# Kernel optimization log

Measured on AMD Instinct MI355X. Metric: run time of the kernel, lower is better.

The kernel has to match this reference:

```python
import jax, jax.numpy as jnp
import numpy as np

ALPHA = 32
R = 16
SCALING = ALPHA / R  # 2.0


def setup_inputs() -> dict:
    key = jax.random.key(0)
    k1, k2, k3, k4 = jax.random.split(key, 4)
    B_, S, D = 4, 2048, 4096
    H, r, O = 8, R, 4096
    x = jax.random.normal(k1, (B_, S, D), dtype=jnp.float32)
    A = jax.random.normal(k2, (H, r, D), dtype=jnp.float32) * 0.02   # down-proj per head
    Bm = jax.random.normal(k3, (H, O, r), dtype=jnp.float32) * 0.02  # up-proj per head
    Wr = jax.random.normal(k4, (H, D), dtype=jnp.float32) * 0.02     # router weight
    br = jnp.zeros((H,), dtype=jnp.float32)                          # router bias
    return {"x": x, "A": A, "B": Bm, "Wr": Wr, "br": br}


def reference(x, A, B, Wr, br):
    H = A.shape[0]
    # Router: logits [b, s, h], scores scaled by num_heads
    router_logits = jnp.einsum('bsd,hd->bsh', x, Wr) + br
    scores = H * jax.nn.softmax(router_logits, axis=-1)
    # Per-head low-rank projection: [b, s, h, r]
    low = jnp.einsum('bsd,hrd->bshr', x, A)
    # Fused up-projection + router-weighted combine over heads: [b, s, o]
    out = jnp.einsum('bshr,hor,bsh->bso', low, B, scores)
    return SCALING * out
```

## Files before the change

kernel.cpp:

```cpp
#include <hip/hip_runtime.h>
#include <math.h>

#define D_DIM 4096
#define O_DIM 4096
#define KSPLIT 8

typedef __attribute__((ext_vector_type(8))) short short8;
typedef __attribute__((ext_vector_type(4))) float floatx4;

__device__ inline unsigned short f2bf(float f) {
    union { float f; unsigned u; } v; v.f = f;
    unsigned r = v.u + 0x7FFF + ((v.u >> 16) & 1);
    return (unsigned short)(r >> 16);
}

__global__ __launch_bounds__(256) void k0a_prepW1(const float* __restrict__ A,
                                                  const float* __restrict__ Wr,
                                                  unsigned short* __restrict__ W1bf) {
    int e = (blockIdx.x * 256 + threadIdx.x) * 4;
    int row = e >> 12;
    int col = e & 4095;
    float4 v;
    if (row < 128)      v = *(const float4*)(A + (size_t)row * D_DIM + col);
    else if (row < 136) v = *(const float4*)(Wr + (size_t)(row - 128) * D_DIM + col);
    else                v = make_float4(0.f, 0.f, 0.f, 0.f);
    ushort4 o; o.x = f2bf(v.x); o.y = f2bf(v.y); o.z = f2bf(v.z); o.w = f2bf(v.w);
    *(ushort4*)(W1bf + e) = o;
}

__global__ __launch_bounds__(256) void k0b_prepBt(const float* __restrict__ B,
                                                  unsigned short* __restrict__ Btbf) {
    int e = (blockIdx.x * 256 + threadIdx.x) * 4;
    int o = e >> 7;
    int k = e & 127;
    int h = k >> 4;
    int r = k & 15;
    float4 v = *(const float4*)(B + (size_t)h * (O_DIM * 16) + (size_t)o * 16 + r);
    ushort4 w; w.x = f2bf(v.x); w.y = f2bf(v.y); w.z = f2bf(v.z); w.w = f2bf(v.w);
    *(ushort4*)(Btbf + e) = w;
}

__global__ __launch_bounds__(256) void k1_gemm1(const float* __restrict__ X,
                                                const unsigned short* __restrict__ W1bf,
                                                float* __restrict__ P) {
    __shared__ short Xs[64][72];
    __shared__ short Ws[144][72];
    const int kslice = blockIdx.x & (KSPLIT - 1);
    const int mblk   = blockIdx.x >> 3;
    const int m0     = mblk * 64;
    const int kbase  = kslice * (D_DIM / KSPLIT);
    const int tid  = threadIdx.x;
    const int wave = tid >> 6;
    const int lane = tid & 63;
    const int lrow = lane & 15;
    const int quad = lane >> 4;

    floatx4 acc[9];
    #pragma unroll
    for (int n = 0; n < 9; ++n) acc[n] = (floatx4)(0.f);

    for (int it = 0; it < (D_DIM / KSPLIT) / 64; ++it) {
        const int k0c = kbase + it * 64;
        #pragma unroll
        for (int i = 0; i < 4; ++i) {
            int e   = tid + i * 256;
            int row = e >> 4;
            int c4  = e & 15;
            float4 v = *(const float4*)(X + (size_t)(m0 + row) * D_DIM + k0c + c4 * 4);
            ushort4 o; o.x = f2bf(v.x); o.y = f2bf(v.y); o.z = f2bf(v.z); o.w = f2bf(v.w);
            *(ushort4*)&Xs[row][c4 * 4] = o;
        }
        #pragma unroll
        for (int i = 0; i < 5; ++i) {
            int e = tid + i * 256;
            if (e < 1152) {
                int row = e >> 3;
                int c8  = e & 7;
                uint4 v = *(const uint4*)(W1bf + (size_t)row * D_DIM + k0c + c8 * 8);
                *(uint4*)&Ws[row][c8 * 8] = v;
            }
        }
        __syncthreads();
        #pragma unroll
        for (int ks = 0; ks < 2; ++ks) {
            const int koff = ks * 32 + quad * 8;
            short8 a = *(const short8*)&Xs[wave * 16 + lrow][koff];
            #pragma unroll
            for (int n = 0; n < 9; ++n) {
                short8 b = *(const short8*)&Ws[n * 16 + lrow][koff];
                acc[n] = __builtin_amdgcn_mfma_f32_16x16x32_bf16(a, b, acc[n], 0, 0, 0);
            }
        }
        __syncthreads();
    }

    float* Pk = P + (size_t)kslice * (8192 * 144);
    #pragma unroll
    for (int n = 0; n < 9; ++n) {
        #pragma unroll
        for (int reg = 0; reg < 4; ++reg) {
            int row = m0 + wave * 16 + quad * 4 + reg;
            int col = n * 16 + lrow;
            Pk[(size_t)row * 144 + col] = acc[n][reg];
        }
    }
}

__global__ __launch_bounds__(256) void k15_reduce_softmax(const float* __restrict__ P,
                                                          const float* __restrict__ br,
                                                          unsigned short* __restrict__ W2) {
    __shared__ float S[16][148];
    const int t0  = blockIdx.x * 16;
    const int tid = threadIdx.x;
    #pragma unroll
    for (int i = 0; i < 3; ++i) {
        int e = tid + i * 256;
        if (e < 576) {
            int row = e / 36;
            int c4  = e - row * 36;
            size_t off = (size_t)(t0 + row) * 144 + c4 * 4;
            float4 s = *(const float4*)(P + off);
            #pragma unroll
            for (int p = 1; p < KSPLIT; ++p) {
                float4 v = *(const float4*)(P + (size_t)p * (8192 * 144) + off);
                s.x += v.x; s.y += v.y; s.z += v.z; s.w += v.w;
            }
            *(float4*)&S[row][c4 * 4] = s;
        }
    }
    __syncthreads();
    if (tid < 16) {
        float l[8]; float m = -1e30f;
        #pragma unroll
        for (int h = 0; h < 8; ++h) { l[h] = S[tid][128 + h] + br[h]; m = fmaxf(m, l[h]); }
        float s = 0.f;
        #pragma unroll
        for (int h = 0; h < 8; ++h) { l[h] = __expf(l[h] - m); s += l[h]; }
        float inv = 16.0f / s;
        #pragma unroll
        for (int h = 0; h < 8; ++h) S[tid][136 + h] = l[h] * inv;
    }
    __syncthreads();
    #pragma unroll
    for (int i = 0; i < 2; ++i) {
        int e   = tid + i * 256;
        int tok = e >> 5;
        int c4  = e & 31;
        int col = c4 * 4;
        float sc = S[tok][136 + (col >> 4)];
        ushort4 o;
        o.x = f2bf(S[tok][col + 0] * sc);
        o.y = f2bf(S[tok][col + 1] * sc);
        o.z = f2bf(S[tok][col + 2] * sc);
        o.w = f2bf(S[tok][col + 3] * sc);
        *(ushort4*)(W2 + (size_t)(t0 + tok) * 128 + col) = o;
    }
}

__global__ __launch_bounds__(256) void k2_gemm2(const unsigned short* __restrict__ W2,
                                                const unsigned short* __restrict__ Btbf,
                                                float* __restrict__ out) {
    __shared__ short Bs[128][136];
    const int nblk = blockIdx.x & 31;
    const int mblk = blockIdx.x >> 5;
    const int m0 = mblk * 128, n0 = nblk * 128;
    const int tid  = threadIdx.x;
    const int wave = tid >> 6;
    const int lane = tid & 63;
    const int lrow = lane & 15;
    const int quad = lane >> 4;

    #pragma unroll
    for (int i = 0; i < 8; ++i) {
        int e   = tid + i * 256;
        int row = e >> 4;
        int c8  = e & 15;
        *(uint4*)&Bs[row][c8 * 8] = *(const uint4*)(Btbf + (size_t)(n0 + row) * 128 + c8 * 8);
    }
    __syncthreads();

    floatx4 acc[2][8];
    #pragma unroll
    for (int i = 0; i < 2; ++i)
        #pragma unroll
        for (int n = 0; n < 8; ++n) acc[i][n] = (floatx4)(0.f);

    #pragma unroll
    for (int ks = 0; ks < 4; ++ks) {
        const int koff = ks * 32 + quad * 8;
        short8 a[2];
        #pragma unroll
        for (int i = 0; i < 2; ++i)
            a[i] = *(const short8*)(W2 + (size_t)(m0 + wave * 32 + i * 16 + lrow) * 128 + koff);
        #pragma unroll
        for (int n = 0; n < 8; ++n) {
            short8 b = *(const short8*)&Bs[n * 16 + lrow][koff];
            #pragma unroll
            for (int i = 0; i < 2; ++i)
                acc[i][n] = __builtin_amdgcn_mfma_f32_16x16x32_bf16(a[i], b, acc[i][n], 0, 0, 0);
        }
    }

    #pragma unroll
    for (int i = 0; i < 2; ++i) {
        #pragma unroll
        for (int n = 0; n < 8; ++n) {
            #pragma unroll
            for (int reg = 0; reg < 4; ++reg) {
                int row = m0 + wave * 32 + i * 16 + quad * 4 + reg;
                int col = n0 + n * 16 + lrow;
                __builtin_nontemporal_store(acc[i][n][reg], out + (size_t)row * O_DIM + col);
            }
        }
    }
}

extern "C" void kernel_launch(void* const* d_in, const int* in_sizes, int n_in,
                              void* d_out, int out_size, void* d_ws, size_t ws_size,
                              hipStream_t stream) {
    const float* x  = (const float*)d_in[0];
    const float* A  = (const float*)d_in[1];
    const float* B  = (const float*)d_in[2];
    const float* Wr = (const float*)d_in[3];
    const float* br = (const float*)d_in[4];
    float* out = (float*)d_out;

    float* ws = (float*)d_ws;
    float*          P     = ws;
    unsigned short* W2    = (unsigned short*)(ws + 9437184);
    unsigned short* W1bf  = (unsigned short*)(ws + 9437184 + 524288);
    unsigned short* Btbf  = (unsigned short*)(ws + 9437184 + 524288 + 294912);

    k0a_prepW1<<<dim3(576), dim3(256), 0, stream>>>(A, Wr, W1bf);
    k0b_prepBt<<<dim3(512), dim3(256), 0, stream>>>(B, Btbf);
    k1_gemm1<<<dim3(128 * KSPLIT), dim3(256), 0, stream>>>(x, W1bf, P);
    k15_reduce_softmax<<<dim3(512), dim3(256), 0, stream>>>(P, br, W2);
    k2_gemm2<<<dim3(64 * 32), dim3(256), 0, stream>>>(W2, Btbf, out);
}
```

Measured before the change: 289.2 us.

## Fuse router GEMM, softmax and up-projection into one per-token-block kernel

Replaces the split-K GEMM1, global partial-sum reduction and separate GEMM2 with a single kernel. Each 512-thread block owns 16 tokens, its 8 waves split K, and the partial sums are reduced in shared memory before the softmax-scaled weights feed the up-projection. Output is staged through LDS so it can be written with vectorized nontemporal stores. The two prep kernels are merged into one launch. This removes the large fp32 partial buffer round-trip and two launches. In exchange, operands are read directly from global memory without LDS tiling, which raises L2 traffic for W1 and B. Each block also reads a shared 16-token x tile, which may under-use the MFMA units.

```diff
diff --git a/kernel.cpp b/kernel.cpp
--- a/kernel.cpp
+++ b/kernel.cpp
@@ -1,9 +1,9 @@
 #include <hip/hip_runtime.h>
+#include <hip/hip_bf16.h>
 #include <math.h>
 
 #define D_DIM 4096
 #define O_DIM 4096
-#define KSPLIT 8
 
 typedef __attribute__((ext_vector_type(8))) short short8;
 typedef __attribute__((ext_vector_type(4))) float floatx4;
@@ -14,203 +14,153 @@
     return (unsigned short)(r >> 16);
 }
 
-__global__ __launch_bounds__(256) void k0a_prepW1(const float* __restrict__ A,
-                                                  const float* __restrict__ Wr,
-                                                  unsigned short* __restrict__ W1bf) {
-    int e = (blockIdx.x * 256 + threadIdx.x) * 4;
-    int row = e >> 12;
-    int col = e & 4095;
-    float4 v;
-    if (row < 128)      v = *(const float4*)(A + (size_t)row * D_DIM + col);
-    else if (row < 136) v = *(const float4*)(Wr + (size_t)(row - 128) * D_DIM + col);
-    else                v = make_float4(0.f, 0.f, 0.f, 0.f);
-    ushort4 o; o.x = f2bf(v.x); o.y = f2bf(v.y); o.z = f2bf(v.z); o.w = f2bf(v.w);
-    *(ushort4*)(W1bf + e) = o;
+__device__ inline unsigned cvt2(float lo, float hi) {
+    __hip_bfloat162 h2 = __float22bfloat162_rn(make_float2(lo, hi));
+    union { __hip_bfloat162 h; unsigned u; } c; c.h = h2;
+    return c.u;
 }
 
-__global__ __launch_bounds__(256) void k0b_prepBt(const float* __restrict__ B,
-                                                  unsigned short* __restrict__ Btbf) {
-    int e = (blockIdx.x * 256 + threadIdx.x) * 4;
-    int o = e >> 7;
-    int k = e & 127;
-    int h = k >> 4;
-    int r = k & 15;
-    float4 v = *(const float4*)(B + (size_t)h * (O_DIM * 16) + (size_t)o * 16 + r);
-    ushort4 w; w.x = f2bf(v.x); w.y = f2bf(v.y); w.z = f2bf(v.z); w.w = f2bf(v.w);
-    *(ushort4*)(Btbf + e) = w;
+__global__ __launch_bounds__(256) void k0_prep(const float* __restrict__ A,
+                                               const float* __restrict__ Wr,
+                                               const float* __restrict__ B,
+                                               unsigned short* __restrict__ W1bf,
+                                               unsigned short* __restrict__ Btbf) {
+    if (blockIdx.x < 576) {
+        int e = (blockIdx.x * 256 + threadIdx.x) * 4;
+        int row = e >> 12;
+        int col = e & 4095;
+        float4 v;
+        if (row < 128)      v = *(const float4*)(A + (size_t)row * D_DIM + col);
+        else if (row < 136) v = *(const float4*)(Wr + (size_t)(row - 128) * D_DIM + col);
+        else                v = make_float4(0.f, 0.f, 0.f, 0.f);
+        ushort4 o; o.x = f2bf(v.x); o.y = f2bf(v.y); o.z = f2bf(v.z); o.w = f2bf(v.w);
+        *(ushort4*)(W1bf + e) = o;
+    } else {
+        int e = ((blockIdx.x - 576) * 256 + threadIdx.x) * 4;
+        int o = e >> 7;
+        int k = e & 127;
+        int h = k >> 4;
+        int r = k & 15;
+        float4 v = *(const float4*)(B + (size_t)h * (O_DIM * 16) + (size_t)o * 16 + r);
+        ushort4 w; w.x = f2bf(v.x); w.y = f2bf(v.y); w.z = f2bf(v.z); w.w = f2bf(v.w);
+        *(ushort4*)(Btbf + e) = w;
+    }
 }
 
-__global__ __launch_bounds__(256) void k1_gemm1(const float* __restrict__ X,
-                                                const unsigned short* __restrict__ W1bf,
-                                                float* __restrict__ P) {
-    __shared__ short Xs[64][72];
-    __shared__ short Ws[144][72];
-    const int kslice = blockIdx.x & (KSPLIT - 1);
-    const int mblk   = blockIdx.x >> 3;
-    const int m0     = mblk * 64;
-    const int kbase  = kslice * (D_DIM / KSPLIT);
+__global__ __launch_bounds__(512, 4) void kf_fused(const float* __restrict__ X,
+                                                   const unsigned short* __restrict__ W1bf,
+                                                   const unsigned short* __restrict__ Btbf,
+                                                   const float* __restrict__ br,
+                                                   float* __restrict__ out) {
+    __shared__ float Sred[8][16][144];
+    __shared__ unsigned short W2s[16][132];
     const int tid  = threadIdx.x;
     const int wave = tid >> 6;
     const int lane = tid & 63;
     const int lrow = lane & 15;
     const int quad = lane >> 4;
+    const int m0   = blockIdx.x * 16;
 
+    const int kb = wave * 512;
     floatx4 acc[9];
     #pragma unroll
     for (int n = 0; n < 9; ++n) acc[n] = (floatx4)(0.f);
 
-    for (int it = 0; it < (D_DIM / KSPLIT) / 64; ++it) {
-        const int k0c = kbase + it * 64;
+    const float*          xrow  = X    + (size_t)(m0 + lrow) * D_DIM + kb + quad * 8;
+    const unsigned short* wbase = W1bf + (size_t)lrow * D_DIM + kb + quad * 8;
+
+    #pragma unroll 2
+    for (int ks = 0; ks < 16; ++ks) {
+        float4 x0 = *(const float4*)(xrow + ks * 32);
+        float4 x1 = *(const float4*)(xrow + ks * 32 + 4);
+        union { unsigned u[4]; short8 s; } a;
+        a.u[0] = cvt2(x0.x, x0.y); a.u[1] = cvt2(x0.z, x0.w);
+        a.u[2] = cvt2(x1.x, x1.y); a.u[3] = cvt2(x1.z, x1.w);
         #pragma unroll
-        for (int i = 0; i < 4; ++i) {
-            int e   = tid + i * 256;
-            int row = e >> 4;
-            int c4  = e & 15;
-            float4 v = *(const float4*)(X + (size_t)(m0 + row) * D_DIM + k0c + c4 * 4);
-            ushort4 o; o.x = f2bf(v.x); o.y = f2bf(v.y); o.z = f2bf(v.z); o.w = f2bf(v.w);
-            *(ushort4*)&Xs[row][c4 * 4] = o;
+        for (int n = 0; n < 9; ++n) {
+            short8 b = *(const short8*)(wbase + (size_t)n * (16 * D_DIM) + ks * 32);
+            acc[n] = __builtin_amdgcn_mfma_f32_16x16x32_bf16(a.s, b, acc[n], 0, 0, 0);
         }
-        #pragma unroll
-        for (int i = 0; i < 5; ++i) {
-            int e = tid + i * 256;
-            if (e < 1152) {
-                int row = e >> 3;
-                int c8  = e & 7;
-                uint4 v = *(const uint4*)(W1bf + (size_t)row * D_DIM + k0c + c8 * 8);
-                *(uint4*)&Ws[row][c8 * 8] = v;
-            }
-        }
-        __syncthreads();
-        #pragma unroll
-        for (int ks = 0; ks < 2; ++ks) {
-            const int koff = ks * 32 + quad * 8;
-            short8 a = *(const short8*)&Xs[wave * 16 + lrow][koff];
-            #pragma unroll
-            for (int n = 0; n < 9; ++n) {
-                short8 b = *(const short8*)&Ws[n * 16 + lrow][koff];
-                acc[n] = __builtin_amdgcn_mfma_f32_16x16x32_bf16(a, b, acc[n], 0, 0, 0);
-            }
-        }
-        __syncthreads();
     }
 
-    float* Pk = P + (size_t)kslice * (8192 * 144);
     #pragma unroll
-    for (int n = 0; n < 9; ++n) {
+    for (int n = 0; n < 9; ++n)
         #pragma unroll
-        for (int reg = 0; reg < 4; ++reg) {
-            int row = m0 + wave * 16 + quad * 4 + reg;
-            int col = n * 16 + lrow;
-            Pk[(size_t)row * 144 + col] = acc[n][reg];
-        }
-    }
-}
+        for (int reg = 0; reg < 4; ++reg)
+            Sred[wave][quad * 4 + reg][n * 16 + lrow] = acc[n][reg];
+    __syncthreads();
 
-__global__ __launch_bounds__(256) void k15_reduce_softmax(const float* __restrict__ P,
-                                                          const float* __restrict__ br,
-                                                          unsigned short* __restrict__ W2) {
-    __shared__ float S[16][148];
-    const int t0  = blockIdx.x * 16;
-    const int tid = threadIdx.x;
-    #pragma unroll
-    for (int i = 0; i < 3; ++i) {
-        int e = tid + i * 256;
-        if (e < 576) {
-            int row = e / 36;
-            int c4  = e - row * 36;
-            size_t off = (size_t)(t0 + row) * 144 + c4 * 4;
-            float4 s = *(const float4*)(P + off);
-            #pragma unroll
-            for (int p = 1; p < KSPLIT; ++p) {
-                float4 v = *(const float4*)(P + (size_t)p * (8192 * 144) + off);
-                s.x += v.x; s.y += v.y; s.z += v.z; s.w += v.w;
-            }
-            *(float4*)&S[row][c4 * 4] = s;
-        }
+    for (int idx = tid; idx < 2304; idx += 512) {
+        int row = idx / 144;
+        int col = idx - row * 144;
+        float s = Sred[0][row][col];
+        #pragma unroll
+        for (int p = 1; p < 8; ++p) s += Sred[p][row][col];
+        Sred[0][row][col] = s;
     }
     __syncthreads();
+
     if (tid < 16) {
         float l[8]; float m = -1e30f;
         #pragma unroll
-        for (int h = 0; h < 8; ++h) { l[h] = S[tid][128 + h] + br[h]; m = fmaxf(m, l[h]); }
+        for (int h = 0; h < 8; ++h) { l[h] = Sred[0][tid][128 + h] + br[h]; m = fmaxf(m, l[h]); }
         float s = 0.f;
         #pragma unroll
         for (int h = 0; h < 8; ++h) { l[h] = __expf(l[h] - m); s += l[h]; }
         float inv = 16.0f / s;
         #pragma unroll
-        for (int h = 0; h < 8; ++h) S[tid][136 + h] = l[h] * inv;
-    }
-    __syncthreads();
-    #pragma unroll
-    for (int i = 0; i < 2; ++i) {
-        int e   = tid + i * 256;
-        int tok = e >> 5;
-        int c4  = e & 31;
-        int col = c4 * 4;
-        float sc = S[tok][136 + (col >> 4)];
-        ushort4 o;
-        o.x = f2bf(S[tok][col + 0] * sc);
-        o.y = f2bf(S[tok][col + 1] * sc);
-        o.z = f2bf(S[tok][col + 2] * sc);
-        o.w = f2bf(S[tok][col + 3] * sc);
-        *(ushort4*)(W2 + (size_t)(t0 + tok) * 128 + col) = o;
-    }
-}
-
-__global__ __launch_bounds__(256) void k2_gemm2(const unsigned short* __restrict__ W2,
-                                                const unsigned short* __restrict__ Btbf,
-                                                float* __restrict__ out) {
-    __shared__ short Bs[128][136];
-    const int nblk = blockIdx.x & 31;
-    const int mblk = blockIdx.x >> 5;
-    const int m0 = mblk * 128, n0 = nblk * 128;
-    const int tid  = threadIdx.x;
-    const int wave = tid >> 6;
-    const int lane = tid & 63;
-    const int lrow = lane & 15;
-    const int quad = lane >> 4;
-
-    #pragma unroll
-    for (int i = 0; i < 8; ++i) {
-        int e   = tid + i * 256;
-        int row = e >> 4;
-        int c8  = e & 15;
-        *(uint4*)&Bs[row][c8 * 8] = *(const uint4*)(Btbf + (size_t)(n0 + row) * 128 + c8 * 8);
+        for (int h = 0; h < 8; ++h) Sred[0][tid][136 + h] = l[h] * inv;
     }
     __syncthreads();
 
-    floatx4 acc[2][8];
+    {
+        int row = tid >> 5;
+        int c   = (tid & 31) * 4;
+        float sc = Sred[0][row][136 + (c >> 4)];
+        float4 v = *(const float4*)&Sred[0][row][c];
+        ushort4 o;
+        o.x = f2bf(v.x * sc); o.y = f2bf(v.y * sc);
+        o.z = f2bf(v.z * sc); o.w = f2bf(v.w * sc);
+        *(ushort4*)&W2s[row][c] = o;
+    }
+    __syncthreads();
+
+    float* bounce = &Sred[0][0][0] + wave * (16 * 132);
+
+    short8 afr[4];
     #pragma unroll
-    for (int i = 0; i < 2; ++i)
+    for (int ks = 0; ks < 4; ++ks)
+        afr[ks] = *(const short8*)&W2s[lrow][ks * 32 + quad * 8];
+
+    const int nb = wave * 512;
+    for (int nc = 0; nc < 4; ++nc) {
+        const int n0c = nb + nc * 128;
+        floatx4 acc2[8];
         #pragma unroll
-        for (int n = 0; n < 8; ++n) acc[i][n] = (floatx4)(0.f);
+        for (int n = 0; n < 8; ++n) acc2[n] = (floatx4)(0.f);
 
-    #pragma unroll
-    for (int ks = 0; ks < 4; ++ks) {
-        const int koff = ks * 32 + quad * 8;
-        short8 a[2];
         #pragma unroll
-        for (int i = 0; i < 2; ++i)
-            a[i] = *(const short8*)(W2 + (size_t)(m0 + wave * 32 + i * 16 + lrow) * 128 + koff);
+        for (int ks = 0; ks < 4; ++ks)
+            #pragma unroll
+            for (int n = 0; n < 8; ++n) {
+                short8 b = *(const short8*)(Btbf + (size_t)(n0c + n * 16 + lrow) * 128 + ks * 32 + quad * 8);
+                acc2[n] = __builtin_amdgcn_mfma_f32_16x16x32_bf16(afr[ks], b, acc2[n], 0, 0, 0);
+            }
+
         #pragma unroll
-        for (int n = 0; n < 8; ++n) {
-            short8 b = *(const short8*)&Bs[n * 16 + lrow][koff];
+        for (int n = 0; n < 8; ++n)
             #pragma unroll
-            for (int i = 0; i < 2; ++i)
-                acc[i][n] = __builtin_amdgcn_mfma_f32_16x16x32_bf16(a[i], b, acc[i][n], 0, 0, 0);
-        }
-    }
+            for (int reg = 0; reg < 4; ++reg)
+                bounce[(quad * 4 + reg) * 132 + n * 16 + lrow] = acc2[n][reg];
 
-    #pragma unroll
-    for (int i = 0; i < 2; ++i) {
         #pragma unroll
-        for (int n = 0; n < 8; ++n) {
-            #pragma unroll
-            for (int reg = 0; reg < 4; ++reg) {
-                int row = m0 + wave * 32 + i * 16 + quad * 4 + reg;
-                int col = n0 + n * 16 + lrow;
-                __builtin_nontemporal_store(acc[i][n][reg], out + (size_t)row * O_DIM + col);
-            }
+        for (int i = 0; i < 8; ++i) {
+            int idx = lane + i * 64;
+            int row = idx >> 5;
+            int u   = idx & 31;
+            floatx4 v = *(const floatx4*)&bounce[row * 132 + u * 4];
+            __builtin_nontemporal_store(v,
+                (floatx4*)(out + (size_t)(m0 + row) * O_DIM + n0c + u * 4));
         }
     }
 }
@@ -225,15 +175,9 @@
     const float* br = (const float*)d_in[4];
     float* out = (float*)d_out;
 
-    float* ws = (float*)d_ws;
-    float*          P     = ws;
-    unsigned short* W2    = (unsigned short*)(ws + 9437184);
-    unsigned short* W1bf  = (unsigned short*)(ws + 9437184 + 524288);
-    unsigned short* Btbf  = (unsigned short*)(ws + 9437184 + 524288 + 294912);
+    unsigned short* W1bf = (unsigned short*)d_ws;
+    unsigned short* Btbf = W1bf + 589824;
 
-    k0a_prepW1<<<dim3(576), dim3(256), 0, stream>>>(A, Wr, W1bf);
-    k0b_prepBt<<<dim3(512), dim3(256), 0, stream>>>(B, Btbf);
-    k1_gemm1<<<dim3(128 * KSPLIT), dim3(256), 0, stream>>>(x, W1bf, P);
-    k15_reduce_softmax<<<dim3(512), dim3(256), 0, stream>>>(P, br, W2);
-    k2_gemm2<<<dim3(64 * 32), dim3(256), 0, stream>>>(W2, Btbf, out);
+    k0_prep<<<dim3(1088), dim3(256), 0, stream>>>(A, Wr, B, W1bf, Btbf);
+    kf_fused<<<dim3(512), dim3(512), 0, stream>>>(x, W1bf, Btbf, br, out);
 }
```

Result: slower. 331.6 us (+14.7%).
